# Performance work log

Measured on AMD Instinct MI355X. Metric: run time of the kernel, lower is better.

Reference implementation:

```python
import jax, jax.numpy as jnp
import numpy as np

H = 2048          # hidden_size
NH = 16           # num attention heads
NKV = 4           # num kv heads (GQA)
HD = 128          # head_dim (= v_head_dim)
E = 16            # n_routed_experts
K = 4             # num_experts_per_tok
DFF = 1024        # moe_intermediate_size
G = 4             # n_group
TG = 2            # topk_group
THETA = 1000000.0
EPS = 1e-6
B, S = 1, 1024


def _rmsnorm(x, w):
    return x * jax.lax.rsqrt(jnp.mean(x * x, axis=-1, keepdims=True) + EPS) * w


def _rope(pos, x):
    # neox-style rotary, full head_dim. x: [B,S,h,HD], pos: [B,S]
    half = HD // 2
    inv_freq = 1.0 / (THETA ** (jnp.arange(half, dtype=jnp.float32) / half))
    ang = pos[..., None].astype(jnp.float32) * inv_freq          # [B,S,half]
    cos = jnp.cos(ang)[:, :, None, :]
    sin = jnp.sin(ang)[:, :, None, :]
    x1, x2 = x[..., :half], x[..., half:]
    return jnp.concatenate([x1 * cos - x2 * sin, x2 * cos + x1 * sin], axis=-1)


def setup_inputs() -> dict:
    key = jax.random.key(0)
    ks = jax.random.split(key, 10)
    sc = 0.02
    return {
        "hidden_states": jax.random.normal(ks[0], (B, S, H), dtype=jnp.float32),
        "positions": jnp.arange(B * S, dtype=jnp.int64 if jax.config.jax_enable_x64 else jnp.int32).reshape(B, S),
        "in_norm_w": jnp.ones((H,), jnp.float32),
        "post_norm_w": jnp.ones((H,), jnp.float32),
        "qkv_w": jax.random.normal(ks[1], (H, (NH + 2 * NKV) * HD), jnp.float32) * sc,
        "o_w": jax.random.normal(ks[2], (NH * HD, H), jnp.float32) * sc,
        "gate_w": jax.random.normal(ks[3], (E, H), jnp.float32) * sc,
        "gate_bias": jax.random.normal(ks[4], (E,), jnp.float32) * sc,
        "gate_up_w": jax.random.normal(ks[5], (E, H, 2 * DFF), jnp.float32) * sc,
        "down_w": jax.random.normal(ks[6], (E, DFF, H), jnp.float32) * sc,
    }


def reference(hidden_states, positions, in_norm_w, post_norm_w, qkv_w, o_w,
              gate_w, gate_bias, gate_up_w, down_w):
    Bq, Sq, _ = hidden_states.shape
    T = Bq * Sq

    # ---- pre-norm attention ----
    residual = hidden_states
    h = _rmsnorm(hidden_states, in_norm_w)
    qkv = h @ qkv_w                                             # [B,S,(NH+2*NKV)*HD]
    q, k, v = jnp.split(qkv, [NH * HD, (NH + NKV) * HD], axis=-1)
    q = q.reshape(Bq, Sq, NH, HD)
    k = k.reshape(Bq, Sq, NKV, HD)
    v = v.reshape(Bq, Sq, NKV, HD)
    q = _rope(positions, q)
    k = _rope(positions, k)
    rep = NH // NKV
    k = jnp.repeat(k, rep, axis=2)                              # [B,S,NH,HD]
    v = jnp.repeat(v, rep, axis=2)
    scores = jnp.einsum('bqhd,bkhd->bhqk', q, k) * (HD ** -0.5)
    causal = jnp.tril(jnp.ones((Sq, Sq), bool))
    scores = jnp.where(causal, scores, -1e30)
    attn = jax.nn.softmax(scores, axis=-1)
    o = jnp.einsum('bhqk,bkhd->bqhd', attn, v).reshape(Bq, Sq, NH * HD)
    h = residual + o @ o_w

    # ---- pre-norm MoE ----
    residual = h
    x = _rmsnorm(h, post_norm_w).reshape(T, H)

    # gate (fp32), sigmoid scores + correction bias, grouped top-k (noaux_tc)
    logits = x.astype(jnp.float32) @ gate_w.T                   # [T,E]
    sig = jax.nn.sigmoid(logits)
    sb = sig + gate_bias.astype(jnp.float32)
    grp = sb.reshape(T, G, E // G)
    group_scores = jax.lax.top_k(grp, 2)[0].sum(-1)             # [T,G]
    _, gidx = jax.lax.top_k(group_scores, TG)
    gmask = jax.nn.one_hot(gidx, G, dtype=sb.dtype).sum(1)      # [T,G]
    emask = jnp.repeat(gmask, E // G, axis=1)                   # [T,E]
    masked = jnp.where(emask > 0, sb, -jnp.inf)
    _, tidx = jax.lax.top_k(masked, K)                          # [T,K]
    w = jnp.take_along_axis(sig, tidx, axis=1)
    w = w / (w.sum(-1, keepdims=True) + 1e-20)                  # renormalize

    # experts: dense compute, sparse combine
    gu = jnp.einsum('td,edf->etf', x, gate_up_w)                # [E,T,2*DFF]
    g, u = jnp.split(gu, 2, axis=-1)
    act = jax.nn.silu(g) * u
    y = jnp.einsum('etf,efd->etd', act, down_w)                 # [E,T,H]
    cw = jnp.zeros((T, E), jnp.float32).at[jnp.arange(T)[:, None], tidx].add(w)
    moe_out = jnp.einsum('te,etd->td', cw, y.astype(jnp.float32))
    return residual + moe_out.astype(hidden_states.dtype).reshape(Bq, Sq, H)
```

## Files before the change

### kernel.cpp

```cpp
#include <hip/hip_runtime.h>
#include <hip/hip_bf16.h>
#include <math.h>

#define H_DIM   2048
#define NH      16
#define NKV     4
#define HD      128
#define NE      16
#define TOPK    4
#define DFF     1024
#define NG      4
#define SEQ     1024
#define QKV_N   3072
#define EPS_RMS 1e-6f
#define THETA   1000000.0f

typedef __attribute__((ext_vector_type(8))) short bf16x8;
typedef __attribute__((ext_vector_type(4))) short s16x4;
typedef __attribute__((ext_vector_type(4))) float f32x4;

__device__ inline unsigned short f2bf(float x) {
    unsigned u = __builtin_bit_cast(unsigned, x);
    unsigned r = (u + 0x7FFFu + ((u >> 16) & 1u)) >> 16;
    return (unsigned short)r;
}

__device__ inline unsigned pk2bf(float lo, float hi) {
    __hip_bfloat162 h = __float22bfloat162_rn(float2{lo, hi});
    unsigned r;
    __builtin_memcpy(&r, &h, 4);
    return r;
}

__global__ __launch_bounds__(256) void w2bfT(const float* __restrict__ in,
                                             unsigned short* __restrict__ out,
                                             int K, int N) {
    const float* src = in + (size_t)blockIdx.z * K * N;
    unsigned short* dst = out + (size_t)blockIdx.z * K * N;
    int n0 = blockIdx.x * 64, k0 = blockIdx.y * 64;
    __shared__ unsigned short tile[64][66];
    int tid = threadIdx.x, c = tid & 63, r4 = tid >> 6;
    #pragma unroll
    for (int rep = 0; rep < 16; rep++) {
        int r = rep * 4 + r4;
        tile[r][c] = f2bf(src[(size_t)(k0 + r) * N + n0 + c]);
    }
    __syncthreads();
    #pragma unroll
    for (int rep = 0; rep < 16; rep++) {
        int r = rep * 4 + r4;
        dst[(size_t)(n0 + r) * K + k0 + c] = tile[c][r];
    }
}

__global__ __launch_bounds__(256) void rmsnorm_dual(const float* __restrict__ in,
                                                    const float* __restrict__ w,
                                                    float* __restrict__ outf,
                                                    unsigned short* __restrict__ outb) {
    int t = blockIdx.x;
    const float* xt = in + (size_t)t * H_DIM;
    float ss = 0.f;
    for (int d = threadIdx.x * 4; d < H_DIM; d += 1024) {
        float4 v = *reinterpret_cast<const float4*>(xt + d);
        ss += v.x * v.x + v.y * v.y + v.z * v.z + v.w * v.w;
    }
    for (int off = 1; off < 64; off <<= 1) ss += __shfl_xor(ss, off);
    __shared__ float red[4];
    __shared__ float srms;
    if ((threadIdx.x & 63) == 0) red[threadIdx.x >> 6] = ss;
    __syncthreads();
    if (threadIdx.x == 0)
        srms = rsqrtf((red[0] + red[1] + red[2] + red[3]) * (1.f / H_DIM) + EPS_RMS);
    __syncthreads();
    float r = srms;
    for (int d = threadIdx.x * 4; d < H_DIM; d += 1024) {
        float4 v  = *reinterpret_cast<const float4*>(xt + d);
        float4 wv = *reinterpret_cast<const float4*>(w + d);
        float4 ov;
        ov.x = v.x * r * wv.x; ov.y = v.y * r * wv.y;
        ov.z = v.z * r * wv.z; ov.w = v.w * r * wv.w;
        if (outf) *reinterpret_cast<float4*>(outf + (size_t)t * H_DIM + d) = ov;
        if (outb) {
            s16x4 bv = (s16x4){(short)f2bf(ov.x), (short)f2bf(ov.y),
                               (short)f2bf(ov.z), (short)f2bf(ov.w)};
            *reinterpret_cast<s16x4*>(outb + (size_t)t * H_DIM + d) = bv;
        }
    }
}

__global__ __launch_bounds__(128) void gemm_qkv_rope(const unsigned short* __restrict__ A,
                                                     const unsigned short* __restrict__ Bt,
                                                     const int* __restrict__ positions,
                                                     unsigned short* __restrict__ Qb,
                                                     unsigned short* __restrict__ Kb,
                                                     unsigned short* __restrict__ Vt) {
    __shared__ unsigned short As[8][66][8];
    __shared__ unsigned short Bs[8][130][8];
    int xb = blockIdx.x;
    int row0 = blockIdx.y * 64, col0 = xb * 128;
    int t = threadIdx.x;
    int w = t >> 6, lane = t & 63, lo = lane & 15, g = lane >> 4;
    int wr = w * 32;
    f32x4 acc[2][8];
    #pragma unroll
    for (int mi = 0; mi < 2; mi++)
        #pragma unroll
        for (int ni = 0; ni < 8; ni++) acc[mi][ni] = (f32x4){0.f, 0.f, 0.f, 0.f};
    int arow8 = t >> 3, ac = t & 7;
    size_t aoff[4], boff[8];
    #pragma unroll
    for (int rep = 0; rep < 4; rep++)
        aoff[rep] = (size_t)(row0 + rep * 16 + arow8) * H_DIM + ac * 8;
    #pragma unroll
    for (int rep = 0; rep < 8; rep++)
        boff[rep] = (size_t)(col0 + rep * 16 + arow8) * H_DIM + ac * 8;
    bf16x8 aR[4], bR[8];
    #pragma unroll
    for (int rep = 0; rep < 4; rep++) aR[rep] = *(const bf16x8*)(A + aoff[rep]);
    #pragma unroll
    for (int rep = 0; rep < 8; rep++) bR[rep] = *(const bf16x8*)(Bt + boff[rep]);
    for (int k0 = 0; k0 < H_DIM; k0 += 64) {
        #pragma unroll
        for (int rep = 0; rep < 4; rep++)
            *(bf16x8*)As[ac][rep * 16 + arow8] = aR[rep];
        #pragma unroll
        for (int rep = 0; rep < 8; rep++)
            *(bf16x8*)Bs[ac][rep * 16 + arow8] = bR[rep];
        int kn = k0 + 64;
        if (kn < H_DIM) {
            #pragma unroll
            for (int rep = 0; rep < 4; rep++) aR[rep] = *(const bf16x8*)(A + aoff[rep] + kn);
            #pragma unroll
            for (int rep = 0; rep < 8; rep++) bR[rep] = *(const bf16x8*)(Bt + boff[rep] + kn);
        }
        __syncthreads();
        #pragma unroll
        for (int kh = 0; kh < 2; kh++) {
            bf16x8 af[2], bfr[8];
            #pragma unroll
            for (int mi = 0; mi < 2; mi++) af[mi] = *(const bf16x8*)As[kh * 4 + g][wr + mi * 16 + lo];
            #pragma unroll
            for (int ni = 0; ni < 8; ni++) bfr[ni] = *(const bf16x8*)Bs[kh * 4 + g][ni * 16 + lo];
            #pragma unroll
            for (int mi = 0; mi < 2; mi++)
                #pragma unroll
                for (int ni = 0; ni < 8; ni++)
                    acc[mi][ni] = __builtin_amdgcn_mfma_f32_16x16x32_bf16(af[mi], bfr[ni], acc[mi][ni], 0, 0, 0);
        }
        __syncthreads();
    }
    if (xb < NH + NKV) {
        bool isQ = (xb < NH);
        unsigned short* dst = isQ ? (Qb + (size_t)xb * SEQ * HD)
                                  : (Kb + (size_t)(xb - NH) * SEQ * HD);
        float qs = isQ ? 0.08838834764831845f : 1.0f;
        float invf[4];
        #pragma unroll
        for (int ni = 0; ni < 4; ni++)
            invf[ni] = __powf(THETA, -(float)(ni * 16 + lo) * (1.0f / 64.0f));
        #pragma unroll
        for (int mi = 0; mi < 2; mi++)
            #pragma unroll
            for (int r = 0; r < 4; r++) {
                int tok = row0 + wr + mi * 16 + g * 4 + r;
                float pos = (float)positions[tok];
                #pragma unroll
                for (int ni = 0; ni < 4; ni++) {
                    float s, c;
                    __sincosf(pos * invf[ni], &s, &c);
                    float x1 = acc[mi][ni][r], x2 = acc[mi][ni + 4][r];
                    int d = ni * 16 + lo;
                    dst[(size_t)tok * HD + d]      = f2bf((x1 * c - x2 * s) * qs);
                    dst[(size_t)tok * HD + d + 64] = f2bf((x2 * c + x1 * s) * qs);
                }
            }
    } else {
        int kvh = xb - (NH + NKV);
        #pragma unroll
        for (int mi = 0; mi < 2; mi++)
            #pragma unroll
            for (int ni = 0; ni < 8; ni++) {
                int tok0 = row0 + wr + mi * 16 + g * 4;
                int d = ni * 16 + lo;
                ushort4 v4;
                v4.x = f2bf(acc[mi][ni][0]);
                v4.y = f2bf(acc[mi][ni][1]);
                v4.z = f2bf(acc[mi][ni][2]);
                v4.w = f2bf(acc[mi][ni][3]);
                *reinterpret_cast<ushort4*>(Vt + ((size_t)kvh * HD + d) * SEQ + tok0) = v4;
            }
    }
}

__global__ __launch_bounds__(256) void gemm_bf16(const unsigned short* __restrict__ A,
                                                 const unsigned short* __restrict__ Bt,
                                                 float* __restrict__ C,
                                                 float* __restrict__ C2,
                                                 const float* __restrict__ R,
                                                 int M, int N, int K) {
    __shared__ unsigned short As[8][130][8];
    __shared__ unsigned short Bs[8][66][8];
    int row0 = blockIdx.y * 128, col0 = blockIdx.x * 64;
    int t = threadIdx.x;
    int w = t >> 6, lane = t & 63, lo = lane & 15, g = lane >> 4;
    int wr = (w >> 1) * 64, wc = (w & 1) * 32;
    f32x4 acc[4][2];
    #pragma unroll
    for (int mi = 0; mi < 4; mi++)
        #pragma unroll
        for (int ni = 0; ni < 2; ni++) acc[mi][ni] = (f32x4){0.f, 0.f, 0.f, 0.f};
    int arow8 = t >> 3, ac = t & 7;
    size_t aoff[4], boff[2];
    #pragma unroll
    for (int rep = 0; rep < 4; rep++)
        aoff[rep] = (size_t)(row0 + rep * 32 + arow8) * K + ac * 8;
    #pragma unroll
    for (int rep = 0; rep < 2; rep++)
        boff[rep] = (size_t)(col0 + rep * 32 + arow8) * K + ac * 8;
    bf16x8 aR[4], bR[2];
    #pragma unroll
    for (int rep = 0; rep < 4; rep++) aR[rep] = *(const bf16x8*)(A + aoff[rep]);
    #pragma unroll
    for (int rep = 0; rep < 2; rep++) bR[rep] = *(const bf16x8*)(Bt + boff[rep]);
    for (int k0 = 0; k0 < K; k0 += 64) {
        #pragma unroll
        for (int rep = 0; rep < 4; rep++)
            *(bf16x8*)As[ac][rep * 32 + arow8] = aR[rep];
        #pragma unroll
        for (int rep = 0; rep < 2; rep++)
            *(bf16x8*)Bs[ac][rep * 32 + arow8] = bR[rep];
        int kn = k0 + 64;
        if (kn < K) {
            #pragma unroll
            for (int rep = 0; rep < 4; rep++) aR[rep] = *(const bf16x8*)(A + aoff[rep] + kn);
            #pragma unroll
            for (int rep = 0; rep < 2; rep++) bR[rep] = *(const bf16x8*)(Bt + boff[rep] + kn);
        }
        __syncthreads();
        #pragma unroll
        for (int kh = 0; kh < 2; kh++) {
            bf16x8 af[4], bfr[2];
            #pragma unroll
            for (int mi = 0; mi < 4; mi++) af[mi] = *(const bf16x8*)As[kh * 4 + g][wr + mi * 16 + lo];
            #pragma unroll
            for (int ni = 0; ni < 2; ni++) bfr[ni] = *(const bf16x8*)Bs[kh * 4 + g][wc + ni * 16 + lo];
            #pragma unroll
            for (int mi = 0; mi < 4; mi++)
                #pragma unroll
                for (int ni = 0; ni < 2; ni++)
                    acc[mi][ni] = __builtin_amdgcn_mfma_f32_16x16x32_bf16(af[mi], bfr[ni], acc[mi][ni], 0, 0, 0);
        }
        __syncthreads();
    }
    #pragma unroll
    for (int mi = 0; mi < 4; mi++)
        #pragma unroll
        for (int ni = 0; ni < 2; ni++)
            #pragma unroll
            for (int r = 0; r < 4; r++) {
                int row = row0 + wr + mi * 16 + g * 4 + r;
                int col = col0 + wc + ni * 16 + lo;
                size_t idx = (size_t)row * N + col;
                float v = acc[mi][ni][r];
                if (R)  v += R[idx];
                C[idx] = v;
                if (C2) C2[idx] = v;
            }
}

__global__ __launch_bounds__(64) void attn_mfma(const unsigned short* __restrict__ Qb,
                                                const unsigned short* __restrict__ Kb,
                                                const unsigned short* __restrict__ Vt,
                                                unsigned short* __restrict__ ob) {
    int qt = blockIdx.x;
    int h  = blockIdx.y;
    int kvh = h >> 2;
    int q0 = qt * 16;
    int l = threadIdx.x;
    int lo = l & 15, g = l >> 4;

    __shared__ alignas(16) unsigned short pbuf[16][40];

    bf16x8 qf[4];
    const unsigned short* qp = Qb + ((size_t)h * SEQ + q0 + lo) * HD + g * 8;
    #pragma unroll
    for (int ks = 0; ks < 4; ks++)
        qf[ks] = *(const bf16x8*)(qp + ks * 32);

    f32x4 accO[8];
    #pragma unroll
    for (int nd = 0; nd < 8; nd++) accO[nd] = (f32x4){0.f, 0.f, 0.f, 0.f};
    float mrun[4], lrun[4];
    #pragma unroll
    for (int r = 0; r < 4; r++) { mrun[r] = -INFINITY; lrun[r] = 0.f; }

    int nc = (q0 + 16 + 31) / 32;
    for (int ch = 0; ch < nc; ch++) {
        int kv0 = ch * 32;
        f32x4 accS[2];
        accS[0] = (f32x4){0.f, 0.f, 0.f, 0.f};
        accS[1] = (f32x4){0.f, 0.f, 0.f, 0.f};
        const unsigned short* kp = Kb + ((size_t)kvh * SEQ + kv0 + lo) * HD + g * 8;
        #pragma unroll
        for (int n = 0; n < 2; n++) {
            const unsigned short* kpn = kp + (size_t)n * 16 * HD;
            #pragma unroll
            for (int ks = 0; ks < 4; ks++) {
                bf16x8 kf = *(const bf16x8*)(kpn + ks * 32);
                accS[n] = __builtin_amdgcn_mfma_f32_16x16x32_bf16(qf[ks], kf, accS[n], 0, 0, 0);
            }
        }
        if (ch == nc - 1) {
            #pragma unroll
            for (int n = 0; n < 2; n++)
                #pragma unroll
                for (int r = 0; r < 4; r++) {
                    int kv = kv0 + n * 16 + lo;
                    int q  = q0 + g * 4 + r;
                    if (kv > q) accS[n][r] = -1e30f;
                }
        }
        float mt[4], fac[4];
        #pragma unroll
        for (int r = 0; r < 4; r++) {
            float m = fmaxf(accS[0][r], accS[1][r]);
            #pragma unroll
            for (int off = 1; off < 16; off <<= 1) m = fmaxf(m, __shfl_xor(m, off));
            mt[r] = fmaxf(mrun[r], m);
            fac[r] = __expf(mrun[r] - mt[r]);
        }
        float psum[4] = {0.f, 0.f, 0.f, 0.f};
        #pragma unroll
        for (int n = 0; n < 2; n++)
            #pragma unroll
            for (int r = 0; r < 4; r++) {
                float p = __expf(accS[n][r] - mt[r]);
                psum[r] += p;
                pbuf[g * 4 + r][n * 16 + lo] = f2bf(p);
            }
        #pragma unroll
        for (int r = 0; r < 4; r++) {
            float s = psum[r];
            #pragma unroll
            for (int off = 1; off < 16; off <<= 1) s += __shfl_xor(s, off);
            lrun[r] = lrun[r] * fac[r] + s;
            mrun[r] = mt[r];
        }
        #pragma unroll
        for (int nd = 0; nd < 8; nd++)
            #pragma unroll
            for (int r = 0; r < 4; r++) accO[nd][r] *= fac[r];
        __builtin_amdgcn_sched_barrier(0);
        bf16x8 pf = *(const bf16x8*)(&pbuf[lo][g * 8]);
        const unsigned short* vp = Vt + ((size_t)kvh * HD + lo) * SEQ + kv0 + g * 8;
        #pragma unroll
        for (int nd = 0; nd < 8; nd++) {
            bf16x8 vf = *(const bf16x8*)(vp + (size_t)nd * 16 * SEQ);
            accO[nd] = __builtin_amdgcn_mfma_f32_16x16x32_bf16(pf, vf, accO[nd], 0, 0, 0);
        }
        __builtin_amdgcn_sched_barrier(0);
    }
    float inv[4];
    #pragma unroll
    for (int r = 0; r < 4; r++) inv[r] = 1.0f / lrun[r];
    #pragma unroll
    for (int nd = 0; nd < 8; nd++)
        #pragma unroll
        for (int r = 0; r < 4; r++)
            ob[(size_t)(q0 + g * 4 + r) * H_DIM + h * HD + nd * 16 + lo] = f2bf(accO[nd][r] * inv[r]);
}

__global__ __launch_bounds__(256) void router_kernel(const float* __restrict__ x,
                                                     const float* __restrict__ gate_w,
                                                     const float* __restrict__ gate_bias,
                                                     int* __restrict__ toklist,
                                                     float* __restrict__ tokw,
                                                     int* __restrict__ cnt) {
    int t = blockIdx.x;
    const float* xt = x + (size_t)t * H_DIM;
    __shared__ float logits[NE];
    __shared__ float red[4];
    for (int e = 0; e < NE; e++) {
        float p = 0.f;
        for (int d = threadIdx.x; d < H_DIM; d += 256) p += xt[d] * gate_w[(size_t)e * H_DIM + d];
        for (int off = 1; off < 64; off <<= 1) p += __shfl_xor(p, off);
        if ((threadIdx.x & 63) == 0) red[threadIdx.x >> 6] = p;
        __syncthreads();
        if (threadIdx.x == 0) logits[e] = red[0] + red[1] + red[2] + red[3];
        __syncthreads();
    }
    if (threadIdx.x == 0) {
        float sig[NE], sb[NE];
        for (int e = 0; e < NE; e++) {
            sig[e] = 1.f / (1.f + expf(-logits[e]));
            sb[e] = sig[e] + gate_bias[e];
        }
        float gs[NG];
        for (int g = 0; g < NG; g++) {
            float m1 = -1e30f, m2 = -1e30f;
            for (int i = 0; i < 4; i++) {
                float v = sb[g * 4 + i];
                if (v > m1) { m2 = m1; m1 = v; } else if (v > m2) m2 = v;
            }
            gs[g] = m1 + m2;
        }
        int g1 = 0;
        for (int g = 1; g < NG; g++) if (gs[g] > gs[g1]) g1 = g;
        int g2 = -1;
        for (int g = 0; g < NG; g++) {
            if (g == g1) continue;
            if (g2 < 0 || gs[g] > gs[g2]) g2 = g;
        }
        bool allowed[NE], used[NE];
        for (int e = 0; e < NE; e++) { int g = e >> 2; allowed[e] = (g == g1 || g == g2); used[e] = false; }
        int sel[TOPK]; float wsel[TOPK]; float wsum = 0.f;
        for (int k = 0; k < TOPK; k++) {
            int best = -1; float bv = -1e30f;
            for (int e = 0; e < NE; e++) {
                if (!allowed[e] || used[e]) continue;
                if (best < 0 || sb[e] > bv) { best = e; bv = sb[e]; }
            }
            used[best] = true; sel[k] = best; wsel[k] = sig[best]; wsum += sig[best];
        }
        float invs = 1.f / (wsum + 1e-20f);
        for (int k = 0; k < TOPK; k++) {
            int e = sel[k];
            int slot = atomicAdd(&cnt[e], 1);
            toklist[e * SEQ + slot] = t;
            tokw[e * SEQ + slot] = wsel[k] * invs;
        }
    }
}

__global__ void prefix_kernel(const int* __restrict__ cnt, int* __restrict__ base) {
    if (threadIdx.x == 0) {
        int s = 0;
        for (int e = 0; e < NE; e++) { base[e] = s; s += cnt[e]; }
    }
}

__global__ __launch_bounds__(256, 2) void moe_gemm1_mfma(const unsigned short* __restrict__ xb,
                                                         const float* __restrict__ gup,
                                                         const int* __restrict__ toklist,
                                                         const int* __restrict__ cnt,
                                                         const int* __restrict__ base,
                                                         unsigned short* __restrict__ act) {
    int e = blockIdx.z;
    int ce = cnt[e];
    int t0 = blockIdx.y * 256;
    if (t0 >= ce) return;
    int f0 = blockIdx.x * 32;
    __shared__ unsigned short As[8][258][8];
    __shared__ unsigned short BsG[8][33][8];
    __shared__ unsigned short BsU[8][33][8];
    __shared__ int toks[256];
    int t = threadIdx.x;
    { int s = t0 + t; toks[t] = toklist[e * SEQ + (s < ce ? s : 0)]; }
    __syncthreads();
    int w = t >> 6, lane = t & 63, lo = lane & 15, g = lane >> 4;
    int wrb = w * 64;
    f32x4 accG[4][2], accU[4][2];
    #pragma unroll
    for (int mi = 0; mi < 4; mi++)
        #pragma unroll
        for (int ni = 0; ni < 2; ni++) {
            accG[mi][ni] = (f32x4){0.f, 0.f, 0.f, 0.f};
            accU[mi][ni] = (f32x4){0.f, 0.f, 0.f, 0.f};
        }
    int arow8 = t >> 3, ac = t & 7;
    size_t abase[8];
    #pragma unroll
    for (int rep = 0; rep < 8; rep++)
        abase[rep] = (size_t)toks[rep * 32 + arow8] * H_DIM + ac * 8;
    int half = t >> 7, tt = t & 127;
    int rp = tt >> 3, nq = tt & 7;
    int kgB = rp >> 2, wq = (rp & 3) * 2;
    unsigned short (*Bsel)[33][8] = half ? BsU : BsG;
    const float* W = gup + (size_t)e * H_DIM * (2 * DFF);
    const float* pB0 = W + (size_t)(2 * rp) * (2 * DFF) + half * DFF + f0 + nq * 4;
    bf16x8 aR[8];
    #pragma unroll
    for (int rep = 0; rep < 8; rep++) aR[rep] = *(const bf16x8*)(xb + abase[rep]);
    f32x4 bR0 = *(const f32x4*)pB0;
    f32x4 bR1 = *(const f32x4*)(pB0 + 2 * DFF);
    f32x4 bR2 = *(const f32x4*)(pB0 + (size_t)32 * 2 * DFF);
    f32x4 bR3 = *(const f32x4*)(pB0 + (size_t)33 * 2 * DFF);
    for (int k0 = 0; k0 < H_DIM; k0 += 64) {
        #pragma unroll
        for (int rep = 0; rep < 8; rep++)
            *(bf16x8*)As[ac][rep * 32 + arow8] = aR[rep];
        #pragma unroll
        for (int j = 0; j < 4; j++) {
            *(unsigned*)&Bsel[kgB][nq * 4 + j][wq]     = pk2bf(bR0[j], bR1[j]);
            *(unsigned*)&Bsel[kgB + 4][nq * 4 + j][wq] = pk2bf(bR2[j], bR3[j]);
        }
        int kn = k0 + 64;
        if (kn < H_DIM) {
            #pragma unroll
            for (int rep = 0; rep < 8; rep++)
                aR[rep] = *(const bf16x8*)(xb + abase[rep] + kn);
            const float* pB = pB0 + (size_t)kn * (2 * DFF);
            bR0 = *(const f32x4*)pB;
            bR1 = *(const f32x4*)(pB + 2 * DFF);
            bR2 = *(const f32x4*)(pB + (size_t)32 * 2 * DFF);
            bR3 = *(const f32x4*)(pB + (size_t)33 * 2 * DFF);
        }
        __syncthreads();
        #pragma unroll
        for (int kh = 0; kh < 2; kh++) {
            bf16x8 af[4], bg[2], bu[2];
            #pragma unroll
            for (int mi = 0; mi < 4; mi++) af[mi] = *(const bf16x8*)As[kh * 4 + g][wrb + mi * 16 + lo];
            #pragma unroll
            for (int ni = 0; ni < 2; ni++) {
                bg[ni] = *(const bf16x8*)BsG[kh * 4 + g][ni * 16 + lo];
                bu[ni] = *(const bf16x8*)BsU[kh * 4 + g][ni * 16 + lo];
            }
            #pragma unroll
            for (int mi = 0; mi < 4; mi++)
                #pragma unroll
                for (int ni = 0; ni < 2; ni++) {
                    accG[mi][ni] = __builtin_amdgcn_mfma_f32_16x16x32_bf16(af[mi], bg[ni], accG[mi][ni], 0, 0, 0);
                    accU[mi][ni] = __builtin_amdgcn_mfma_f32_16x16x32_bf16(af[mi], bu[ni], accU[mi][ni], 0, 0, 0);
                }
        }
        __syncthreads();
    }
    int b = base[e];
    #pragma unroll
    for (int mi = 0; mi < 4; mi++)
        #pragma unroll
        for (int ni = 0; ni < 2; ni++)
            #pragma unroll
            for (int r = 0; r < 4; r++) {
                int slot = t0 + wrb + mi * 16 + g * 4 + r;
                if (slot < ce) {
                    float gv = accG[mi][ni][r], uv = accU[mi][ni][r];
                    float a = (gv / (1.f + __expf(-gv))) * uv;
                    act[(size_t)(b + slot) * DFF + f0 + ni * 16 + lo] = f2bf(a);
                }
            }
}

__global__ __launch_bounds__(256, 4) void moe_gemm2_mfma(const unsigned short* __restrict__ act,
                                                         const float* __restrict__ down,
                                                         const int* __restrict__ toklist,
                                                         const float* __restrict__ tokw,
                                                         const int* __restrict__ cnt,
                                                         const int* __restrict__ base,
                                                         float* __restrict__ out) {
    int e = blockIdx.z;
    int ce = cnt[e];
    int t0 = blockIdx.y * 256;
    if (t0 >= ce) return;
    int c0 = blockIdx.x * 32;
    __shared__ unsigned short As[8][258][8];
    __shared__ unsigned short Bs[8][33][8];
    int t = threadIdx.x;
    int w = t >> 6, lane = t & 63, lo = lane & 15, g = lane >> 4;
    int wrb = w * 64;
    int b = base[e];
    f32x4 acc[4][2];
    #pragma unroll
    for (int mi = 0; mi < 4; mi++)
        #pragma unroll
        for (int ni = 0; ni < 2; ni++) acc[mi][ni] = (f32x4){0.f, 0.f, 0.f, 0.f};
    int arow8 = t >> 3, ac = t & 7;
    size_t abase[8];
    #pragma unroll
    for (int rep = 0; rep < 8; rep++) {
        int slot = t0 + rep * 32 + arow8;
        abase[rep] = (size_t)(b + (slot < ce ? slot : t0)) * DFF + ac * 8;
    }
    int tt = t & 127;
    int rp = tt >> 3, nq = tt & 7;
    int kgB = rp >> 2, wq = (rp & 3) * 2;
    const float* pB0 = down + (size_t)e * DFF * H_DIM + (size_t)(2 * rp) * H_DIM + c0 + nq * 4;
    bool stageB = (t < 128);
    bf16x8 aR[8];
    #pragma unroll
    for (int rep = 0; rep < 8; rep++) aR[rep] = *(const bf16x8*)(act + abase[rep]);
    f32x4 bR0 = (f32x4){0.f,0.f,0.f,0.f}, bR1 = bR0, bR2 = bR0, bR3 = bR0;
    if (stageB) {
        bR0 = *(const f32x4*)pB0;
        bR1 = *(const f32x4*)(pB0 + H_DIM);
        bR2 = *(const f32x4*)(pB0 + (size_t)32 * H_DIM);
        bR3 = *(const f32x4*)(pB0 + (size_t)33 * H_DIM);
    }
    for (int k0 = 0; k0 < DFF; k0 += 64) {
        #pragma unroll
        for (int rep = 0; rep < 8; rep++)
            *(bf16x8*)As[ac][rep * 32 + arow8] = aR[rep];
        if (stageB) {
            #pragma unroll
            for (int j = 0; j < 4; j++) {
                *(unsigned*)&Bs[kgB][nq * 4 + j][wq]     = pk2bf(bR0[j], bR1[j]);
                *(unsigned*)&Bs[kgB + 4][nq * 4 + j][wq] = pk2bf(bR2[j], bR3[j]);
            }
        }
        int kn = k0 + 64;
        if (kn < DFF) {
            #pragma unroll
            for (int rep = 0; rep < 8; rep++)
                aR[rep] = *(const bf16x8*)(act + abase[rep] + kn);
            if (stageB) {
                const float* pB = pB0 + (size_t)kn * H_DIM;
                bR0 = *(const f32x4*)pB;
                bR1 = *(const f32x4*)(pB + H_DIM);
                bR2 = *(const f32x4*)(pB + (size_t)32 * H_DIM);
                bR3 = *(const f32x4*)(pB + (size_t)33 * H_DIM);
            }
        }
        __syncthreads();
        #pragma unroll
        for (int kh = 0; kh < 2; kh++) {
            bf16x8 af[4], bfr[2];
            #pragma unroll
            for (int mi = 0; mi < 4; mi++) af[mi] = *(const bf16x8*)As[kh * 4 + g][wrb + mi * 16 + lo];
            #pragma unroll
            for (int ni = 0; ni < 2; ni++) bfr[ni] = *(const bf16x8*)Bs[kh * 4 + g][ni * 16 + lo];
            #pragma unroll
            for (int mi = 0; mi < 4; mi++)
                #pragma unroll
                for (int ni = 0; ni < 2; ni++)
                    acc[mi][ni] = __builtin_amdgcn_mfma_f32_16x16x32_bf16(af[mi], bfr[ni], acc[mi][ni], 0, 0, 0);
        }
        __syncthreads();
    }
    #pragma unroll
    for (int mi = 0; mi < 4; mi++)
        #pragma unroll
        for (int r = 0; r < 4; r++) {
            int slot = t0 + wrb + mi * 16 + g * 4 + r;
            if (slot < ce) {
                int tok = toklist[e * SEQ + slot];
                float wt = tokw[e * SEQ + slot];
                #pragma unroll
                for (int ni = 0; ni < 2; ni++)
                    atomicAdd(&out[(size_t)tok * H_DIM + c0 + ni * 16 + lo],
                              wt * acc[mi][ni][r]);
            }
        }
}

extern "C" void kernel_launch(void* const* d_in, const int* in_sizes, int n_in,
                              void* d_out, int out_size, void* d_ws, size_t ws_size,
                              hipStream_t stream) {
    const float* hidden     = (const float*)d_in[0];
    const int*   positions  = (const int*)d_in[1];
    const float* in_norm_w  = (const float*)d_in[2];
    const float* post_norm_w= (const float*)d_in[3];
    const float* qkv_w      = (const float*)d_in[4];
    const float* o_w        = (const float*)d_in[5];
    const float* gate_w     = (const float*)d_in[6];
    const float* gate_bias  = (const float*)d_in[7];
    const float* gate_up_w  = (const float*)d_in[8];
    const float* down_w     = (const float*)d_in[9];
    float* out = (float*)d_out;

    float* ws   = (float*)d_ws;
    float* h2   = ws;
    float* x    = h2  + (size_t)SEQ * H_DIM;
    float* tokw = x   + (size_t)SEQ * H_DIM;
    int* toklist = (int*)(tokw + NE * SEQ);
    int* cnt  = toklist + NE * SEQ;
    int* base = cnt + NE;
    unsigned short* hb = (unsigned short*)(base + NE);
    unsigned short* ob = hb + (size_t)SEQ * H_DIM;
    unsigned short* xbuf = ob + (size_t)SEQ * H_DIM;
    unsigned short* act = xbuf + (size_t)SEQ * H_DIM;
    unsigned short* Qb = act + (size_t)4 * SEQ * DFF;
    unsigned short* Kb = Qb + (size_t)NH * SEQ * HD;
    unsigned short* Vt = Kb + (size_t)NKV * SEQ * HD;
    unsigned short* qkvT = Vt + (size_t)NKV * HD * SEQ;
    unsigned short* oT   = qkvT + (size_t)QKV_N * H_DIM;

    w2bfT<<<dim3(QKV_N / 64, H_DIM / 64, 1), 256, 0, stream>>>(qkv_w, qkvT, H_DIM, QKV_N);
    w2bfT<<<dim3(H_DIM / 64, H_DIM / 64, 1), 256, 0, stream>>>(o_w, oT, H_DIM, H_DIM);

    rmsnorm_dual<<<SEQ, 256, 0, stream>>>(hidden, in_norm_w, nullptr, hb);
    gemm_qkv_rope<<<dim3(QKV_N / 128, SEQ / 64), 128, 0, stream>>>(hb, qkvT, positions, Qb, Kb, Vt);
    attn_mfma<<<dim3(SEQ / 16, NH), 64, 0, stream>>>(Qb, Kb, Vt, ob);
    gemm_bf16<<<dim3(H_DIM / 64, SEQ / 128), 256, 0, stream>>>(ob, oT, h2, out, hidden,
                                                               SEQ, H_DIM, H_DIM);
    rmsnorm_dual<<<SEQ, 256, 0, stream>>>(h2, post_norm_w, x, xbuf);
    (void)hipMemsetAsync(cnt, 0, NE * sizeof(int), stream);
    router_kernel<<<SEQ, 256, 0, stream>>>(x, gate_w, gate_bias, toklist, tokw, cnt);
    prefix_kernel<<<1, 64, 0, stream>>>(cnt, base);
    moe_gemm1_mfma<<<dim3(DFF / 32, SEQ / 256, NE), 256, 0, stream>>>(xbuf, gate_up_w, toklist, cnt, base, act);
    moe_gemm2_mfma<<<dim3(H_DIM / 32, SEQ / 256, NE), 256, 0, stream>>>(act, down_w, toklist, tokw, cnt, base, out);
}
```

Before: 446.6 us.

## Pair causal attention tiles per block and deepen MoE GEMM register prefetch

Attention blocks now run two waves that take complementary causal query tiles (qt and its mirror), so each block has a roughly even amount of work and the grid has half as many blocks. Both MoE GEMMs get two register buffers, so global loads are issued two k-steps ahead, giving more latency hiding at the cost of more registers. gemm2's launch-bounds occupancy hint drops from 4 to 2 to leave room for those registers. The risk is lower occupancy and register spills.

```diff
diff --git a/kernel.cpp b/kernel.cpp
--- a/kernel.cpp
+++ b/kernel.cpp
@@ -268,18 +268,20 @@
             }
 }
 
-__global__ __launch_bounds__(64) void attn_mfma(const unsigned short* __restrict__ Qb,
-                                                const unsigned short* __restrict__ Kb,
-                                                const unsigned short* __restrict__ Vt,
-                                                unsigned short* __restrict__ ob) {
-    int qt = blockIdx.x;
+__global__ __launch_bounds__(128) void attn_mfma(const unsigned short* __restrict__ Qb,
+                                                 const unsigned short* __restrict__ Kb,
+                                                 const unsigned short* __restrict__ Vt,
+                                                 unsigned short* __restrict__ ob) {
+    int bx = blockIdx.x;
     int h  = blockIdx.y;
     int kvh = h >> 2;
+    int wid = threadIdx.x >> 6;
+    int qt = wid ? (SEQ / 16 - 1 - bx) : bx;
     int q0 = qt * 16;
-    int l = threadIdx.x;
+    int l = threadIdx.x & 63;
     int lo = l & 15, g = l >> 4;
 
-    __shared__ alignas(16) unsigned short pbuf[16][40];
+    __shared__ alignas(16) unsigned short pbuf[2][16][40];
 
     bf16x8 qf[4];
     const unsigned short* qp = Qb + ((size_t)h * SEQ + q0 + lo) * HD + g * 8;
@@ -336,7 +338,7 @@
             for (int r = 0; r < 4; r++) {
                 float p = __expf(accS[n][r] - mt[r]);
                 psum[r] += p;
-                pbuf[g * 4 + r][n * 16 + lo] = f2bf(p);
+                pbuf[wid][g * 4 + r][n * 16 + lo] = f2bf(p);
             }
         #pragma unroll
         for (int r = 0; r < 4; r++) {
@@ -351,7 +353,7 @@
             #pragma unroll
             for (int r = 0; r < 4; r++) accO[nd][r] *= fac[r];
         __builtin_amdgcn_sched_barrier(0);
-        bf16x8 pf = *(const bf16x8*)(&pbuf[lo][g * 8]);
+        bf16x8 pf = *(const bf16x8*)(&pbuf[wid][lo][g * 8]);
         const unsigned short* vp = Vt + ((size_t)kvh * HD + lo) * SEQ + kv0 + g * 8;
         #pragma unroll
         for (int nd = 0; nd < 8; nd++) {
@@ -478,52 +480,42 @@
     unsigned short (*Bsel)[33][8] = half ? BsU : BsG;
     const float* W = gup + (size_t)e * H_DIM * (2 * DFF);
     const float* pB0 = W + (size_t)(2 * rp) * (2 * DFF) + half * DFF + f0 + nq * 4;
-    bf16x8 aR[8];
-    #pragma unroll
-    for (int rep = 0; rep < 8; rep++) aR[rep] = *(const bf16x8*)(xb + abase[rep]);
-    f32x4 bR0 = *(const f32x4*)pB0;
-    f32x4 bR1 = *(const f32x4*)(pB0 + 2 * DFF);
-    f32x4 bR2 = *(const f32x4*)(pB0 + (size_t)32 * 2 * DFF);
-    f32x4 bR3 = *(const f32x4*)(pB0 + (size_t)33 * 2 * DFF);
-    for (int k0 = 0; k0 < H_DIM; k0 += 64) {
-        #pragma unroll
-        for (int rep = 0; rep < 8; rep++)
-            *(bf16x8*)As[ac][rep * 32 + arow8] = aR[rep];
-        #pragma unroll
-        for (int j = 0; j < 4; j++) {
-            *(unsigned*)&Bsel[kgB][nq * 4 + j][wq]     = pk2bf(bR0[j], bR1[j]);
-            *(unsigned*)&Bsel[kgB + 4][nq * 4 + j][wq] = pk2bf(bR2[j], bR3[j]);
-        }
-        int kn = k0 + 64;
-        if (kn < H_DIM) {
-            #pragma unroll
-            for (int rep = 0; rep < 8; rep++)
-                aR[rep] = *(const bf16x8*)(xb + abase[rep] + kn);
-            const float* pB = pB0 + (size_t)kn * (2 * DFF);
-            bR0 = *(const f32x4*)pB;
-            bR1 = *(const f32x4*)(pB + 2 * DFF);
-            bR2 = *(const f32x4*)(pB + (size_t)32 * 2 * DFF);
-            bR3 = *(const f32x4*)(pB + (size_t)33 * 2 * DFF);
-        }
-        __syncthreads();
-        #pragma unroll
-        for (int kh = 0; kh < 2; kh++) {
-            bf16x8 af[4], bg[2], bu[2];
-            #pragma unroll
-            for (int mi = 0; mi < 4; mi++) af[mi] = *(const bf16x8*)As[kh * 4 + g][wrb + mi * 16 + lo];
-            #pragma unroll
-            for (int ni = 0; ni < 2; ni++) {
-                bg[ni] = *(const bf16x8*)BsG[kh * 4 + g][ni * 16 + lo];
-                bu[ni] = *(const bf16x8*)BsU[kh * 4 + g][ni * 16 + lo];
-            }
-            #pragma unroll
-            for (int mi = 0; mi < 4; mi++)
-                #pragma unroll
-                for (int ni = 0; ni < 2; ni++) {
-                    accG[mi][ni] = __builtin_amdgcn_mfma_f32_16x16x32_bf16(af[mi], bg[ni], accG[mi][ni], 0, 0, 0);
-                    accU[mi][ni] = __builtin_amdgcn_mfma_f32_16x16x32_bf16(af[mi], bu[ni], accU[mi][ni], 0, 0, 0);
-                }
-        }
+
+#define G1_LOAD_A(dst, kk) { _Pragma("unroll") \
+    for (int rep = 0; rep < 8; rep++) dst[rep] = *(const bf16x8*)(xb + abase[rep] + (kk)); }
+#define G1_LOAD_B(b0_, b1_, b2_, b3_, kk) { const float* pB = pB0 + (size_t)(kk) * (2 * DFF); \
+    b0_ = *(const f32x4*)pB; b1_ = *(const f32x4*)(pB + 2 * DFF); \
+    b2_ = *(const f32x4*)(pB + (size_t)32 * 2 * DFF); b3_ = *(const f32x4*)(pB + (size_t)33 * 2 * DFF); }
+#define G1_STAGE(aSrc, b0_, b1_, b2_, b3_) { _Pragma("unroll") \
+    for (int rep = 0; rep < 8; rep++) *(bf16x8*)As[ac][rep * 32 + arow8] = aSrc[rep]; \
+    _Pragma("unroll") for (int j = 0; j < 4; j++) { \
+        *(unsigned*)&Bsel[kgB][nq * 4 + j][wq]     = pk2bf(b0_[j], b1_[j]); \
+        *(unsigned*)&Bsel[kgB + 4][nq * 4 + j][wq] = pk2bf(b2_[j], b3_[j]); } }
+#define G1_MFMA() { _Pragma("unroll") for (int kh = 0; kh < 2; kh++) { \
+    bf16x8 af[4], bg[2], bu[2]; \
+    _Pragma("unroll") for (int mi = 0; mi < 4; mi++) af[mi] = *(const bf16x8*)As[kh * 4 + g][wrb + mi * 16 + lo]; \
+    _Pragma("unroll") for (int ni = 0; ni < 2; ni++) { \
+        bg[ni] = *(const bf16x8*)BsG[kh * 4 + g][ni * 16 + lo]; \
+        bu[ni] = *(const bf16x8*)BsU[kh * 4 + g][ni * 16 + lo]; } \
+    _Pragma("unroll") for (int mi = 0; mi < 4; mi++) \
+        _Pragma("unroll") for (int ni = 0; ni < 2; ni++) { \
+            accG[mi][ni] = __builtin_amdgcn_mfma_f32_16x16x32_bf16(af[mi], bg[ni], accG[mi][ni], 0, 0, 0); \
+            accU[mi][ni] = __builtin_amdgcn_mfma_f32_16x16x32_bf16(af[mi], bu[ni], accU[mi][ni], 0, 0, 0); } } }
+
+    bf16x8 aRA[8], aRB[8];
+    f32x4 bA0, bA1, bA2, bA3, bB0, bB1, bB2, bB3;
+    G1_LOAD_A(aRA, 0);  G1_LOAD_B(bA0, bA1, bA2, bA3, 0);
+    G1_LOAD_A(aRB, 64); G1_LOAD_B(bB0, bB1, bB2, bB3, 64);
+    for (int k0 = 0; k0 < H_DIM; k0 += 128) {
+        G1_STAGE(aRA, bA0, bA1, bA2, bA3);
+        if (k0 + 128 < H_DIM) { G1_LOAD_A(aRA, k0 + 128); G1_LOAD_B(bA0, bA1, bA2, bA3, k0 + 128); }
+        __syncthreads();
+        G1_MFMA();
+        __syncthreads();
+        G1_STAGE(aRB, bB0, bB1, bB2, bB3);
+        if (k0 + 192 < H_DIM) { G1_LOAD_A(aRB, k0 + 192); G1_LOAD_B(bB0, bB1, bB2, bB3, k0 + 192); }
+        __syncthreads();
+        G1_MFMA();
         __syncthreads();
     }
     int b = base[e];
@@ -542,7 +534,7 @@
             }
 }
 
-__global__ __launch_bounds__(256, 4) void moe_gemm2_mfma(const unsigned short* __restrict__ act,
+__global__ __launch_bounds__(256, 2) void moe_gemm2_mfma(const unsigned short* __restrict__ act,
                                                          const float* __restrict__ down,
                                                          const int* __restrict__ toklist,
                                                          const float* __restrict__ tokw,
@@ -577,54 +569,40 @@
     int kgB = rp >> 2, wq = (rp & 3) * 2;
     const float* pB0 = down + (size_t)e * DFF * H_DIM + (size_t)(2 * rp) * H_DIM + c0 + nq * 4;
     bool stageB = (t < 128);
-    bf16x8 aR[8];
-    #pragma unroll
-    for (int rep = 0; rep < 8; rep++) aR[rep] = *(const bf16x8*)(act + abase[rep]);
-    f32x4 bR0 = (f32x4){0.f,0.f,0.f,0.f}, bR1 = bR0, bR2 = bR0, bR3 = bR0;
-    if (stageB) {
-        bR0 = *(const f32x4*)pB0;
-        bR1 = *(const f32x4*)(pB0 + H_DIM);
-        bR2 = *(const f32x4*)(pB0 + (size_t)32 * H_DIM);
-        bR3 = *(const f32x4*)(pB0 + (size_t)33 * H_DIM);
-    }
-    for (int k0 = 0; k0 < DFF; k0 += 64) {
-        #pragma unroll
-        for (int rep = 0; rep < 8; rep++)
-            *(bf16x8*)As[ac][rep * 32 + arow8] = aR[rep];
-        if (stageB) {
-            #pragma unroll
-            for (int j = 0; j < 4; j++) {
-                *(unsigned*)&Bs[kgB][nq * 4 + j][wq]     = pk2bf(bR0[j], bR1[j]);
-                *(unsigned*)&Bs[kgB + 4][nq * 4 + j][wq] = pk2bf(bR2[j], bR3[j]);
-            }
-        }
-        int kn = k0 + 64;
-        if (kn < DFF) {
-            #pragma unroll
-            for (int rep = 0; rep < 8; rep++)
-                aR[rep] = *(const bf16x8*)(act + abase[rep] + kn);
-            if (stageB) {
-                const float* pB = pB0 + (size_t)kn * H_DIM;
-                bR0 = *(const f32x4*)pB;
-                bR1 = *(const f32x4*)(pB + H_DIM);
-                bR2 = *(const f32x4*)(pB + (size_t)32 * H_DIM);
-                bR3 = *(const f32x4*)(pB + (size_t)33 * H_DIM);
-            }
-        }
-        __syncthreads();
-        #pragma unroll
-        for (int kh = 0; kh < 2; kh++) {
-            bf16x8 af[4], bfr[2];
-            #pragma unroll
-            for (int mi = 0; mi < 4; mi++) af[mi] = *(const bf16x8*)As[kh * 4 + g][wrb + mi * 16 + lo];
-            #pragma unroll
-            for (int ni = 0; ni < 2; ni++) bfr[ni] = *(const bf16x8*)Bs[kh * 4 + g][ni * 16 + lo];
-            #pragma unroll
-            for (int mi = 0; mi < 4; mi++)
-                #pragma unroll
-                for (int ni = 0; ni < 2; ni++)
-                    acc[mi][ni] = __builtin_amdgcn_mfma_f32_16x16x32_bf16(af[mi], bfr[ni], acc[mi][ni], 0, 0, 0);
-        }
+
+#define G2_LOAD_A(dst, kk) { _Pragma("unroll") \
+    for (int rep = 0; rep < 8; rep++) dst[rep] = *(const bf16x8*)(act + abase[rep] + (kk)); }
+#define G2_LOAD_B(b0_, b1_, b2_, b3_, kk) if (stageB) { const float* pB = pB0 + (size_t)(kk) * H_DIM; \
+    b0_ = *(const f32x4*)pB; b1_ = *(const f32x4*)(pB + H_DIM); \
+    b2_ = *(const f32x4*)(pB + (size_t)32 * H_DIM); b3_ = *(const f32x4*)(pB + (size_t)33 * H_DIM); }
+#define G2_STAGE(aSrc, b0_, b1_, b2_, b3_) { _Pragma("unroll") \
+    for (int rep = 0; rep < 8; rep++) *(bf16x8*)As[ac][rep * 32 + arow8] = aSrc[rep]; \
+    if (stageB) { _Pragma("unroll") for (int j = 0; j < 4; j++) { \
+        *(unsigned*)&Bs[kgB][nq * 4 + j][wq]     = pk2bf(b0_[j], b1_[j]); \
+        *(unsigned*)&Bs[kgB + 4][nq * 4 + j][wq] = pk2bf(b2_[j], b3_[j]); } } }
+#define G2_MFMA() { _Pragma("unroll") for (int kh = 0; kh < 2; kh++) { \
+    bf16x8 af[4], bfr[2]; \
+    _Pragma("unroll") for (int mi = 0; mi < 4; mi++) af[mi] = *(const bf16x8*)As[kh * 4 + g][wrb + mi * 16 + lo]; \
+    _Pragma("unroll") for (int ni = 0; ni < 2; ni++) bfr[ni] = *(const bf16x8*)Bs[kh * 4 + g][ni * 16 + lo]; \
+    _Pragma("unroll") for (int mi = 0; mi < 4; mi++) \
+        _Pragma("unroll") for (int ni = 0; ni < 2; ni++) \
+            acc[mi][ni] = __builtin_amdgcn_mfma_f32_16x16x32_bf16(af[mi], bfr[ni], acc[mi][ni], 0, 0, 0); } }
+
+    bf16x8 aRA[8], aRB[8];
+    f32x4 bA0, bA1, bA2, bA3, bB0, bB1, bB2, bB3;
+    bA0 = bA1 = bA2 = bA3 = bB0 = bB1 = bB2 = bB3 = (f32x4){0.f, 0.f, 0.f, 0.f};
+    G2_LOAD_A(aRA, 0);  G2_LOAD_B(bA0, bA1, bA2, bA3, 0);
+    G2_LOAD_A(aRB, 64); G2_LOAD_B(bB0, bB1, bB2, bB3, 64);
+    for (int k0 = 0; k0 < DFF; k0 += 128) {
+        G2_STAGE(aRA, bA0, bA1, bA2, bA3);
+        if (k0 + 128 < DFF) { G2_LOAD_A(aRA, k0 + 128); G2_LOAD_B(bA0, bA1, bA2, bA3, k0 + 128); }
+        __syncthreads();
+        G2_MFMA();
+        __syncthreads();
+        G2_STAGE(aRB, bB0, bB1, bB2, bB3);
+        if (k0 + 192 < DFF) { G2_LOAD_A(aRB, k0 + 192); G2_LOAD_B(bB0, bB1, bB2, bB3, k0 + 192); }
+        __syncthreads();
+        G2_MFMA();
         __syncthreads();
     }
     #pragma unroll
@@ -680,7 +658,7 @@
 
     rmsnorm_dual<<<SEQ, 256, 0, stream>>>(hidden, in_norm_w, nullptr, hb);
     gemm_qkv_rope<<<dim3(QKV_N / 128, SEQ / 64), 128, 0, stream>>>(hb, qkvT, positions, Qb, Kb, Vt);
-    attn_mfma<<<dim3(SEQ / 16, NH), 64, 0, stream>>>(Qb, Kb, Vt, ob);
+    attn_mfma<<<dim3(SEQ / 32, NH), 128, 0, stream>>>(Qb, Kb, Vt, ob);
     gemm_bf16<<<dim3(H_DIM / 64, SEQ / 128), 256, 0, stream>>>(ob, oT, h2, out, hidden,
                                                                SEQ, H_DIM, H_DIM);
     rmsnorm_dual<<<SEQ, 256, 0, stream>>>(h2, post_norm_w, x, xbuf);
```

Result: slower. 522.7 us (+17.0%).
